# Performance work log

Hardware: AMD Instinct MI355X
Metric: run time of the kernel (lower is better)

## Reference

```python
import jax, jax.numpy as jnp
import numpy as np

B, N, S, D = 32, 128, 64, 512
MAX_LEN = 5000


def make_pe(d_model, max_len):
    pos = np.arange(max_len, dtype=np.float32)[:, None]
    div = np.exp(np.arange(0, d_model, 2, dtype=np.float32) * (-np.log(10000.0) / d_model))
    pe = np.zeros((max_len, d_model), dtype=np.float32)
    pe[:, 0::2] = np.sin(pos * div)
    pe[:, 1::2] = np.cos(pos * div)
    return jnp.asarray(pe)


def setup_inputs() -> dict:
    key = jax.random.key(0)
    ks = jax.random.split(key, 16)
    s1 = 1.0 / np.sqrt(D)
    s2 = 1.0 / np.sqrt(2 * D)
    inp = {
        "x": jax.random.normal(ks[0], (B, N), jnp.float32),
        "timesteps": jax.random.randint(ks[1], (B,), 0, 1000),
        "fusion_feat": jax.random.normal(ks[2], (B, D), jnp.float32),
        "tar_image_feat": jax.random.normal(ks[3], (B, N, S, D), jnp.float32),
        "pe": make_pe(D, MAX_LEN),
        # torch Linear weights are [out, in]
        "Wq": jax.random.normal(ks[4], (D, D), jnp.float32) * s1,
        "Wk": jax.random.normal(ks[5], (D, D), jnp.float32) * s1,
        "Wv": jax.random.normal(ks[6], (D, D), jnp.float32) * s1,
        "Wp": jax.random.normal(ks[7], (D, D), jnp.float32) * s1,
        "bp": jnp.zeros((D,), jnp.float32),
        "Wt1": jax.random.normal(ks[8], (D, D), jnp.float32) * s1,
        "bt1": jnp.zeros((D,), jnp.float32),
        "Wt2": jax.random.normal(ks[9], (D, D), jnp.float32) * s1,
        "bt2": jnp.zeros((D,), jnp.float32),
        "Wd1": jax.random.normal(ks[10], (2 * D, 2 * D), jnp.float32) * s2,
        "bd1": jnp.zeros((2 * D,), jnp.float32),
        "Wd2": jax.random.normal(ks[11], (1, 2 * D), jnp.float32) * s2,
        "bd2": jnp.zeros((1,), jnp.float32),
    }
    return inp


def reference(x, timesteps, fusion_feat, tar_image_feat, pe,
              Wq, Wk, Wv, Wp, bp, Wt1, bt1, Wt2, bt2, Wd1, bd1, Wd2, bd2):
    # timestep embedding: pe[timesteps] -> [B, D], then 2-layer SiLU MLP (eval mode: dropout off)
    cond = jax.nn.silu(pe[timesteps] @ Wt1.T + bt1) @ Wt2.T + bt2  # [B, D]

    # similarity argmax over S tokens, then gather best token per (b, n)
    sim = jnp.einsum('bd,bnsd->bns', fusion_feat, tar_image_feat)  # [B, N, S]
    best = jnp.argmax(sim, axis=-1)                                # [B, N]
    tif = jnp.take_along_axis(tar_image_feat, best[:, :, None, None], axis=2)[:, :, 0, :]  # [B, N, D]

    # single-vector attention over N candidates
    q = (fusion_feat + cond) @ Wq.T                  # [B, D]
    k = (tif + cond[:, None, :]) @ Wk.T              # [B, N, D]
    v = (tif + cond[:, None, :]) @ Wv.T              # [B, N, D]
    w = jax.nn.softmax(jnp.einsum('bd,bnd->bn', q, k) + x, axis=-1)  # [B, N]
    new_emb = jnp.einsum('bn,bnd->bd', w, v) @ Wp.T + bp             # [B, D]

    # MLP decode over concat [new_emb (broadcast), tif]
    emb = jnp.concatenate([jnp.broadcast_to(new_emb[:, None, :], tif.shape), tif], axis=-1)  # [B, N, 2D]
    h = jax.nn.relu(emb @ Wd1.T + bd1)
    p = (h @ Wd2.T + bd2)[..., 0] + w                # [B, N]

    # sort descending along N
    return -jnp.sort(-p, axis=1)
```

## Files before the change

kernel.cpp:

```cpp
#include <hip/hip_runtime.h>
#include <hip/hip_bf16.h>
#include <math.h>


#define BB 32
#define NN 128
#define SS 64
#define DD 512

typedef __attribute__((ext_vector_type(8))) short short8;
typedef __attribute__((ext_vector_type(4))) float f32x4;

__device__ __forceinline__ ushort f2bf(float f) {
    unsigned u = __float_as_uint(f);
    unsigned r = (u + 0x7fffu + ((u >> 16) & 1u)) >> 16;
    return (ushort)r;
}

__device__ __forceinline__ unsigned* flag_at(unsigned* fl, int b, int s) {
    return fl + (size_t)(b * 8 + s) * 16;
}
__device__ __forceinline__ void flag_add(unsigned* f) {
    __syncthreads();
    if (threadIdx.x == 0)
        __hip_atomic_fetch_add(f, 1u, __ATOMIC_RELEASE, __HIP_MEMORY_SCOPE_AGENT);
}
__device__ __forceinline__ void flag_wait(unsigned* f, unsigned target) {
    if (threadIdx.x == 0) {
        while (__hip_atomic_load(f, __ATOMIC_RELAXED, __HIP_MEMORY_SCOPE_AGENT) < target)
            __builtin_amdgcn_s_sleep(4);
        __builtin_amdgcn_fence(__ATOMIC_ACQUIRE, "agent");
    }
    __syncthreads();
}

__global__ __launch_bounds__(256) void k_init(unsigned* __restrict__ flags) {
    flags[blockIdx.x * 256 + threadIdx.x] = 0u;
}

__device__ __forceinline__ void wave_dot512x4(
    const float* __restrict__ w, size_t ldw, float4 xa, float4 xb,
    int lane, float out[4]) {
    float4 ra[4], rb[4];
#pragma unroll
    for (int r = 0; r < 4; ++r) {
        const float4* row = reinterpret_cast<const float4*>(w + (size_t)r * ldw);
        ra[r] = row[lane * 2];
        rb[r] = row[lane * 2 + 1];
    }
#pragma unroll
    for (int r = 0; r < 4; ++r) {
        float s = ra[r].x * xa.x + ra[r].y * xa.y + ra[r].z * xa.z + ra[r].w * xa.w
                + rb[r].x * xb.x + rb[r].y * xb.y + rb[r].z * xb.z + rb[r].w * xb.w;
#pragma unroll
        for (int off = 32; off; off >>= 1) s += __shfl_xor(s, off);
        out[r] = s;
    }
}

__global__ __launch_bounds__(256) void bmv(
    const float* __restrict__ W, int ldw, const float* __restrict__ bias,
    const float* __restrict__ Xa, float* __restrict__ Y, int R, int act) {
    __shared__ __align__(16) float xl[DD];
    int b = blockIdx.y, tid = threadIdx.x, lane = tid & 63, wave = tid >> 6;
    const float* src = Xa + (size_t)b * DD;
    for (int i = tid; i < DD; i += 256) xl[i] = src[i];
    __syncthreads();
    float4 xa = reinterpret_cast<const float4*>(xl)[lane * 2];
    float4 xb = reinterpret_cast<const float4*>(xl)[lane * 2 + 1];
    int j0 = blockIdx.x * 16 + wave * 4;
    float s[4];
    wave_dot512x4(W + (size_t)j0 * ldw, ldw, xa, xb, lane, s);
    if (lane < 4) {
        int j = j0 + lane;
        float v = s[lane];
        if (bias) v += bias[j];
        if (act == 1) v = v / (1.f + expf(-v));
        Y[(size_t)b * R + j] = v;
    }
}

__global__ __launch_bounds__(256) void k2_fused(
    const int* __restrict__ ts, const float* __restrict__ pe,
    const float* __restrict__ fusion, const float* __restrict__ tif,
    const float* __restrict__ Wt1, const float* __restrict__ bt1,
    const float* __restrict__ Wt2, const float* __restrict__ bt2,
    const float* __restrict__ Wq, const float* __restrict__ Wk,
    const float* __restrict__ Wd1, ushort* __restrict__ Wb,
    float* __restrict__ h, float* __restrict__ q,
    float* __restrict__ cond, float* __restrict__ qk,
    float* __restrict__ tif_best, ushort* __restrict__ abf,
    unsigned* __restrict__ flags) {
    __shared__ __align__(16) float xl[DD];
    __shared__ __align__(16) float paux[4][64];
    __shared__ float bv_s[4];
    __shared__ int bi_s[4];
    __shared__ int bidx_s;
    int blk = blockIdx.x, tid = threadIdx.x, lane = tid & 63, wave = tid >> 6;

    if (blk < 256) {
        int b = blk >> 3, part = blk & 7;
        int rows0 = part * 64;
        {
            const float* per = pe + (size_t)ts[b] * DD;
            for (int i = tid; i < DD; i += 256) xl[i] = per[i];
        }
        __syncthreads();
        {
            float4 xa = reinterpret_cast<const float4*>(xl)[lane * 2];
            float4 xb = reinterpret_cast<const float4*>(xl)[lane * 2 + 1];
            for (int j0 = rows0 + wave * 16; j0 < rows0 + wave * 16 + 16; j0 += 4) {
                float s[4];
                wave_dot512x4(Wt1 + (size_t)j0 * DD, DD, xa, xb, lane, s);
                if (lane < 4) {
                    float v = s[lane] + bt1[j0 + lane];
                    h[(size_t)b * DD + j0 + lane] = v / (1.f + expf(-v));
                }
            }
        }
        flag_add(flag_at(flags, b, 0));
        flag_wait(flag_at(flags, b, 0), 8);
        for (int i = tid; i < DD; i += 256) xl[i] = h[(size_t)b * DD + i];
        __syncthreads();
        {
            float4 xa = reinterpret_cast<const float4*>(xl)[lane * 2];
            float4 xb = reinterpret_cast<const float4*>(xl)[lane * 2 + 1];
            for (int j0 = rows0 + wave * 16; j0 < rows0 + wave * 16 + 16; j0 += 4) {
                float s[4];
                wave_dot512x4(Wt2 + (size_t)j0 * DD, DD, xa, xb, lane, s);
                if (lane < 4)
                    cond[(size_t)b * DD + j0 + lane] = s[lane] + bt2[j0 + lane];
            }
        }
        flag_add(flag_at(flags, b, 1));
        flag_wait(flag_at(flags, b, 1), 8);
        for (int i = tid; i < DD; i += 256)
            xl[i] = fusion[(size_t)b * DD + i] + cond[(size_t)b * DD + i];
        __syncthreads();
        {
            float4 xa = reinterpret_cast<const float4*>(xl)[lane * 2];
            float4 xb = reinterpret_cast<const float4*>(xl)[lane * 2 + 1];
            for (int j0 = rows0 + wave * 16; j0 < rows0 + wave * 16 + 16; j0 += 4) {
                float s[4];
                wave_dot512x4(Wq + (size_t)j0 * DD, DD, xa, xb, lane, s);
                if (lane < 4) q[(size_t)b * DD + j0 + lane] = s[lane];
            }
        }
        flag_add(flag_at(flags, b, 2));
        flag_wait(flag_at(flags, b, 2), 8);
        for (int i = tid; i < DD; i += 256) xl[i] = q[(size_t)b * DD + i];
        __syncthreads();
        {
            int c0 = part * 64;
            float p = 0.f;
            for (int j = wave * 128; j < wave * 128 + 128; ++j)
                p += xl[j] * Wk[(size_t)j * DD + c0 + lane];
            paux[wave][lane] = p;
            __syncthreads();
            if (tid < 64)
                qk[(size_t)b * DD + c0 + tid] =
                    paux[0][tid] + paux[1][tid] + paux[2][tid] + paux[3][tid];
        }
        return;
    }

    int bn = blk - 256, b = bn >> 7;
    if (bn < 1024) {
        int idx = (bn * 256 + tid) * 2;
        int r = idx >> 9, k = idx & 511;
        float2 v = *reinterpret_cast<const float2*>(Wd1 + (size_t)r * 1024 + 512 + k);
        ushort2 o = {f2bf(v.x), f2bf(v.y)};
        *reinterpret_cast<ushort2*>(Wb + (size_t)r * 512 + k) = o;
    }
    for (int i = tid; i < DD; i += 256) xl[i] = fusion[(size_t)b * DD + i];
    __syncthreads();
    float4 xa = reinterpret_cast<const float4*>(xl)[lane * 2];
    float4 xb = reinterpret_cast<const float4*>(xl)[lane * 2 + 1];
    const float* base = tif + (size_t)bn * SS * DD;
    float bv = -INFINITY;
    int bi = 0;
    for (int s0 = wave * 16; s0 < wave * 16 + 16; s0 += 4) {
        float sv[4];
        wave_dot512x4(base + (size_t)s0 * DD, DD, xa, xb, lane, sv);
#pragma unroll
        for (int r = 0; r < 4; ++r)
            if (sv[r] > bv) { bv = sv[r]; bi = s0 + r; }
    }
    if (lane == 0) { bv_s[wave] = bv; bi_s[wave] = bi; }
    __syncthreads();
    if (tid == 0) {
        float v = bv_s[0]; int i0 = bi_s[0];
        for (int w = 1; w < 4; w++)
            if (bv_s[w] > v) { v = bv_s[w]; i0 = bi_s[w]; }
        bidx_s = i0;
    }
    __syncthreads();
    const float* src = base + (size_t)bidx_s * DD;
    for (int i = tid; i < DD; i += 256) {
        float vv = src[i];
        tif_best[(size_t)bn * DD + i] = vv;
        abf[(size_t)bn * DD + i] = f2bf(vv);
    }
}

__global__ __launch_bounds__(256) void k_vsum(
    const float* __restrict__ qk, const float* __restrict__ x,
    const float* __restrict__ tif_best, const float* __restrict__ cond,
    float* __restrict__ wout, float* __restrict__ vsum) {
    __shared__ __align__(16) float qkl[DD];
    __shared__ float wl[NN];
    __shared__ float redm[2], reds[2];
    int b = blockIdx.y, tid = threadIdx.x, lane = tid & 63, wave = tid >> 6;
    for (int i = tid; i < DD; i += 256) qkl[i] = qk[(size_t)b * DD + i];
    __syncthreads();
    {
        float4 xa = reinterpret_cast<const float4*>(qkl)[lane * 2];
        float4 xb = reinterpret_cast<const float4*>(qkl)[lane * 2 + 1];
        for (int n0 = wave * 32; n0 < wave * 32 + 32; n0 += 4) {
            float s[4];
            wave_dot512x4(tif_best + ((size_t)(b * NN + n0)) * DD, DD, xa, xb, lane, s);
            if (lane < 4) wl[n0 + lane] = s[lane] + x[b * NN + n0 + lane];
        }
    }
    __syncthreads();
    float v = 0.f;
    if (tid < NN) {
        v = wl[tid];
        float m = v;
#pragma unroll
        for (int off = 32; off; off >>= 1) m = fmaxf(m, __shfl_xor(m, off));
        if (lane == 0) redm[wave] = m;
    }
    __syncthreads();
    float m = fmaxf(redm[0], redm[1]);
    float e = 0.f;
    if (tid < NN) {
        e = expf(v - m);
        float s = e;
#pragma unroll
        for (int off = 32; off; off >>= 1) s += __shfl_xor(s, off);
        if (lane == 0) reds[wave] = s;
    }
    __syncthreads();
    if (tid < NN) wl[tid] = e;
    __syncthreads();
    float inv = 1.f / (reds[0] + reds[1]);
    if (blockIdx.x == 0 && tid < NN) wout[b * NN + tid] = wl[tid] * inv;
    int d = blockIdx.x * 256 + tid;
    const float* base = tif_best + (size_t)b * NN * DD + d;
    float s = 0.f;
#pragma unroll 8
    for (int n = 0; n < NN; n++) s += wl[n] * base[(size_t)n * DD];
    vsum[(size_t)b * DD + d] = s * inv + cond[(size_t)b * DD + d];
}

__global__ __launch_bounds__(256) void k4_mfma(
    const ushort* __restrict__ Abf, const ushort* __restrict__ Wb,
    const float* __restrict__ Wd1, const float* __restrict__ bd1,
    const float* __restrict__ ne, const float* __restrict__ Wd2,
    float* __restrict__ p_part) {
    __shared__ ushort aS[2][128 * 64];
    __shared__ ushort bS[2][128 * 64];
    __shared__ __align__(16) float nel[DD];
    __shared__ float uloc[128];
    int tid = threadIdx.x, l = tid & 63, w = tid >> 6;
    int m0 = blockIdx.x * 128, n0 = blockIdx.y * 128;
    int b = blockIdx.x;
    int wm = w >> 1, wn = w & 1;

    for (int i = tid; i < DD; i += 256) nel[i] = ne[(size_t)b * DD + i];
    __syncthreads();
    float4 na = reinterpret_cast<const float4*>(nel)[l * 2];
    float4 nb = reinterpret_cast<const float4*>(nel)[l * 2 + 1];

#define STAGE(K0, BUF)                                                         \
    {                                                                          \
        _Pragma("unroll") for (int i = 0; i < 4; ++i) {                        \
            int L = i * 4096 + w * 1024 + l * 16;                              \
            int row = L >> 7;                                                  \
            int bo = L & 127;                                                  \
            int sb = bo ^ ((row & 7) << 4);                                    \
            const ushort* ga = Abf + (size_t)(m0 + row) * DD + (K0) + (sb >> 1); \
            const ushort* gb = Wb + (size_t)(n0 + row) * DD + (K0) + (sb >> 1);  \
            __builtin_amdgcn_global_load_lds(                                  \
                (const __attribute__((address_space(1))) void*)ga,             \
                (__attribute__((address_space(3))) void*)(aS[BUF] + i * 2048 + w * 512), \
                16, 0, 0);                                                     \
            __builtin_amdgcn_global_load_lds(                                  \
                (const __attribute__((address_space(1))) void*)gb,             \
                (__attribute__((address_space(3))) void*)(bS[BUF] + i * 2048 + w * 512), \
                16, 0, 0);                                                     \
        }                                                                      \
    }

    STAGE(0, 0);
    for (int j0 = 0; j0 < 32; j0 += 4) {
        int r = w * 32 + j0;
        float s[4];
        wave_dot512x4(Wd1 + (size_t)(n0 + r) * 1024, 1024, na, nb, l, s);
        if (l < 4) uloc[r + l] = s[l] + bd1[n0 + r + l];
    }
    __syncthreads();

    f32x4 acc[4][4];
#pragma unroll
    for (int i = 0; i < 4; i++)
#pragma unroll
        for (int j = 0; j < 4; j++) acc[i][j] = (f32x4){0.f, 0.f, 0.f, 0.f};

    int cur = 0;
    for (int k0 = 0; k0 < DD; k0 += 64) {
        if (k0 + 64 < DD) STAGE(k0 + 64, cur ^ 1);
#pragma unroll
        for (int kk = 0; kk < 2; ++kk) {
            short8 af[4], bf[4];
#pragma unroll
            for (int f = 0; f < 4; ++f) {
                int ra = wm * 64 + f * 16 + (l & 15);
                int boa = (((l >> 4) * 16 + kk * 64)) ^ ((ra & 7) << 4);
                af[f] = *reinterpret_cast<const short8*>(&aS[cur][ra * 64 + (boa >> 1)]);
                int rb = wn * 64 + f * 16 + (l & 15);
                int bob = (((l >> 4) * 16 + kk * 64)) ^ ((rb & 7) << 4);
                bf[f] = *reinterpret_cast<const short8*>(&bS[cur][rb * 64 + (bob >> 1)]);
            }
#pragma unroll
            for (int fm = 0; fm < 4; ++fm)
#pragma unroll
                for (int fn = 0; fn < 4; ++fn)
                    acc[fm][fn] = __builtin_amdgcn_mfma_f32_16x16x32_bf16(
                        af[fm], bf[fn], acc[fm][fn], 0, 0, 0);
        }
        __syncthreads();
        cur ^= 1;
    }
#undef STAGE
#pragma unroll
    for (int fm = 0; fm < 4; ++fm) {
#pragma unroll
        for (int reg = 0; reg < 4; ++reg) {
            float pp = 0.f;
#pragma unroll
            for (int fn = 0; fn < 4; ++fn) {
                int rl = wn * 64 + fn * 16 + (l & 15);
                float hh = acc[fm][fn][reg] + uloc[rl];
                if (hh > 0.f) pp += Wd2[n0 + rl] * hh;
            }
#pragma unroll
            for (int off = 1; off < 16; off <<= 1) pp += __shfl_xor(pp, off);
            if ((l & 15) == 0) {
                int m = m0 + wm * 64 + fm * 16 + (l >> 4) * 4 + reg;
                p_part[(size_t)m * 16 + blockIdx.y * 2 + wn] = pp;
            }
        }
    }
}

__global__ __launch_bounds__(128) void k5_sort(
    const float* __restrict__ p_part, const float* __restrict__ wout,
    const float* __restrict__ bd2, float* __restrict__ out) {
    __shared__ float v[NN];
    int b = blockIdx.x, tid = threadIdx.x;
    int bn = b * NN + tid;
    float s = bd2[0] + wout[bn];
#pragma unroll
    for (int c = 0; c < 16; c++) s += p_part[(size_t)bn * 16 + c];
    v[tid] = s;
    __syncthreads();
    for (int k = 2; k <= NN; k <<= 1) {
        for (int j = k >> 1; j > 0; j >>= 1) {
            int ixj = tid ^ j;
            if (ixj > tid) {
                float a = v[tid], bb2 = v[ixj];
                bool desc = (tid & k) == 0;
                if (desc ? (a < bb2) : (a > bb2)) { v[tid] = bb2; v[ixj] = a; }
            }
            __syncthreads();
        }
    }
    out[bn] = v[tid];
}

extern "C" void kernel_launch(void* const* d_in, const int* in_sizes, int n_in,
                              void* d_out, int out_size, void* d_ws, size_t ws_size,
                              hipStream_t stream) {
    const float* x      = (const float*)d_in[0];
    const int*   ts     = (const int*)d_in[1];
    const float* fusion = (const float*)d_in[2];
    const float* tif    = (const float*)d_in[3];
    const float* pe     = (const float*)d_in[4];
    const float* Wq     = (const float*)d_in[5];
    const float* Wk     = (const float*)d_in[6];
    const float* Wv     = (const float*)d_in[7];
    const float* Wp     = (const float*)d_in[8];
    const float* bp     = (const float*)d_in[9];
    const float* Wt1    = (const float*)d_in[10];
    const float* bt1    = (const float*)d_in[11];
    const float* Wt2    = (const float*)d_in[12];
    const float* bt2    = (const float*)d_in[13];
    const float* Wd1    = (const float*)d_in[14];
    const float* bd1    = (const float*)d_in[15];
    const float* Wd2    = (const float*)d_in[16];
    const float* bd2    = (const float*)d_in[17];

    float* ws = (float*)d_ws;
    float* cond     = ws;
    float* qk       = cond + 16384;
    float* h        = qk + 16384;
    float* q        = h + 16384;
    float* wout     = q + 16384;
    float* vsum     = wout + 4096;
    float* ve       = vsum + 16384;
    float* ne       = ve + 16384;
    float* p_part   = ne + 16384;
    float* tif_best = p_part + 65536;
    ushort* Abf     = (ushort*)(tif_best + 2097152);
    ushort* Wb      = Abf + 2097152;
    unsigned* flags = (unsigned*)(Wb + 524288);
    float* out = (float*)d_out;

    hipLaunchKernelGGL(k_init, dim3(16), dim3(256), 0, stream, flags);

    hipLaunchKernelGGL(k2_fused, dim3(256 + BB * NN), dim3(256), 0, stream,
                       ts, pe, fusion, tif, Wt1, bt1, Wt2, bt2, Wq, Wk,
                       Wd1, Wb, h, q, cond, qk, tif_best, Abf, flags);

    hipLaunchKernelGGL(k_vsum, dim3(2, BB), dim3(256), 0, stream,
                       qk, x, tif_best, cond, wout, vsum);

    hipLaunchKernelGGL(bmv, dim3(32, BB), dim3(256), 0, stream,
                       Wv, DD, nullptr, vsum, ve, DD, 0);
    hipLaunchKernelGGL(bmv, dim3(32, BB), dim3(256), 0, stream,
                       Wp, DD, bp, ve, ne, DD, 0);

    hipLaunchKernelGGL(k4_mfma, dim3(32, 8), dim3(256), 0, stream,
                       Abf, Wb, Wd1, bd1, ne, Wd2, p_part);
    hipLaunchKernelGGL(k5_sort, dim3(BB), dim3(128), 0, stream,
                       p_part, wout, bd2, out);
}
```

Before: 205.0 us.

## Split head MLP into grid-barrier kernel and fuse attention tail with scores

```diff
diff --git a/kernel.cpp b/kernel.cpp
--- a/kernel.cpp
+++ b/kernel.cpp
@@ -17,25 +17,28 @@
     return (ushort)r;
 }
 
-__device__ __forceinline__ unsigned* flag_at(unsigned* fl, int b, int s) {
-    return fl + (size_t)(b * 8 + s) * 16;
-}
-__device__ __forceinline__ void flag_add(unsigned* f) {
-    __syncthreads();
-    if (threadIdx.x == 0)
-        __hip_atomic_fetch_add(f, 1u, __ATOMIC_RELEASE, __HIP_MEMORY_SCOPE_AGENT);
-}
-__device__ __forceinline__ void flag_wait(unsigned* f, unsigned target) {
+__device__ __forceinline__ void bar_sync(unsigned* base, int blk) {
+    __syncthreads();
     if (threadIdx.x == 0) {
-        while (__hip_atomic_load(f, __ATOMIC_RELAXED, __HIP_MEMORY_SCOPE_AGENT) < target)
-            __builtin_amdgcn_s_sleep(4);
+        unsigned* grp = base + (blk >> 5) * 16;
+        if (__hip_atomic_fetch_add(grp, 1u, __ATOMIC_ACQ_REL,
+                                   __HIP_MEMORY_SCOPE_AGENT) == 31u) {
+            if (__hip_atomic_fetch_add(base + 120, 1u, __ATOMIC_ACQ_REL,
+                                       __HIP_MEMORY_SCOPE_AGENT) == 7u) {
+                __hip_atomic_store(base + 124, 1u, __ATOMIC_RELEASE,
+                                   __HIP_MEMORY_SCOPE_AGENT);
+            }
+        }
+        while (__hip_atomic_load(base + 124, __ATOMIC_RELAXED,
+                                 __HIP_MEMORY_SCOPE_AGENT) == 0u)
+            __builtin_amdgcn_s_sleep(2);
         __builtin_amdgcn_fence(__ATOMIC_ACQUIRE, "agent");
     }
     __syncthreads();
 }
 
-__global__ __launch_bounds__(256) void k_init(unsigned* __restrict__ flags) {
-    flags[blockIdx.x * 256 + threadIdx.x] = 0u;
+__global__ __launch_bounds__(256) void k_init(unsigned* __restrict__ bars) {
+    for (int i = threadIdx.x; i < 5 * 128; i += 256) bars[i] = 0u;
 }
 
 __device__ __forceinline__ void wave_dot512x4(
@@ -58,113 +61,96 @@
     }
 }
 
-__global__ __launch_bounds__(256) void bmv(
-    const float* __restrict__ W, int ldw, const float* __restrict__ bias,
-    const float* __restrict__ Xa, float* __restrict__ Y, int R, int act) {
-    __shared__ __align__(16) float xl[DD];
-    int b = blockIdx.y, tid = threadIdx.x, lane = tid & 63, wave = tid >> 6;
-    const float* src = Xa + (size_t)b * DD;
-    for (int i = tid; i < DD; i += 256) xl[i] = src[i];
-    __syncthreads();
-    float4 xa = reinterpret_cast<const float4*>(xl)[lane * 2];
-    float4 xb = reinterpret_cast<const float4*>(xl)[lane * 2 + 1];
-    int j0 = blockIdx.x * 16 + wave * 4;
-    float s[4];
-    wave_dot512x4(W + (size_t)j0 * ldw, ldw, xa, xb, lane, s);
-    if (lane < 4) {
-        int j = j0 + lane;
-        float v = s[lane];
-        if (bias) v += bias[j];
-        if (act == 1) v = v / (1.f + expf(-v));
-        Y[(size_t)b * R + j] = v;
-    }
-}
-
-__global__ __launch_bounds__(256) void k2_fused(
+__global__ __launch_bounds__(256) void k_head(
     const int* __restrict__ ts, const float* __restrict__ pe,
-    const float* __restrict__ fusion, const float* __restrict__ tif,
+    const float* __restrict__ fusion,
     const float* __restrict__ Wt1, const float* __restrict__ bt1,
     const float* __restrict__ Wt2, const float* __restrict__ bt2,
     const float* __restrict__ Wq, const float* __restrict__ Wk,
+    float* __restrict__ h, float* __restrict__ cond,
+    float* __restrict__ q, float* __restrict__ qk,
+    unsigned* __restrict__ bars) {
+    __shared__ __align__(16) float xl[DD];
+    __shared__ float paux[4][64];
+    int blk = blockIdx.x, tid = threadIdx.x, lane = tid & 63, wave = tid >> 6;
+    int b = blk & 31, seg = blk >> 5;
+
+    {
+        const float* per = pe + (size_t)ts[b] * DD;
+        for (int i = tid; i < DD; i += 256) xl[i] = per[i];
+        __syncthreads();
+        float4 xa = reinterpret_cast<const float4*>(xl)[lane * 2];
+        float4 xb = reinterpret_cast<const float4*>(xl)[lane * 2 + 1];
+        for (int j0 = seg * 64 + wave * 16; j0 < seg * 64 + wave * 16 + 16; j0 += 4) {
+            float s[4];
+            wave_dot512x4(Wt1 + (size_t)j0 * DD, DD, xa, xb, lane, s);
+            if (lane < 4) {
+                float v = s[lane] + bt1[j0 + lane];
+                h[(size_t)b * DD + j0 + lane] = v / (1.f + expf(-v));
+            }
+        }
+    }
+    bar_sync(bars + 0 * 128, blk);
+
+    {
+        const float* src = h + (size_t)b * DD;
+        for (int i = tid; i < DD; i += 256) xl[i] = src[i];
+        __syncthreads();
+        float4 xa = reinterpret_cast<const float4*>(xl)[lane * 2];
+        float4 xb = reinterpret_cast<const float4*>(xl)[lane * 2 + 1];
+        for (int j0 = seg * 64 + wave * 16; j0 < seg * 64 + wave * 16 + 16; j0 += 4) {
+            float s[4];
+            wave_dot512x4(Wt2 + (size_t)j0 * DD, DD, xa, xb, lane, s);
+            if (lane < 4)
+                cond[(size_t)b * DD + j0 + lane] = s[lane] + bt2[j0 + lane];
+        }
+    }
+    bar_sync(bars + 1 * 128, blk);
+
+    {
+        for (int i = tid; i < DD; i += 256)
+            xl[i] = fusion[(size_t)b * DD + i] + cond[(size_t)b * DD + i];
+        __syncthreads();
+        float4 xa = reinterpret_cast<const float4*>(xl)[lane * 2];
+        float4 xb = reinterpret_cast<const float4*>(xl)[lane * 2 + 1];
+        for (int j0 = seg * 64 + wave * 16; j0 < seg * 64 + wave * 16 + 16; j0 += 4) {
+            float s[4];
+            wave_dot512x4(Wq + (size_t)j0 * DD, DD, xa, xb, lane, s);
+            if (lane < 4) q[(size_t)b * DD + j0 + lane] = s[lane];
+        }
+    }
+    bar_sync(bars + 2 * 128, blk);
+
+    {
+        const float* src = q + (size_t)b * DD;
+        for (int i = tid; i < DD; i += 256) xl[i] = src[i];
+        __syncthreads();
+        int c0 = seg * 64;
+        float p = 0.f;
+        for (int j = wave * 128; j < wave * 128 + 128; ++j)
+            p += xl[j] * Wk[(size_t)j * DD + c0 + lane];
+        paux[wave][lane] = p;
+        __syncthreads();
+        if (tid < 64)
+            qk[(size_t)b * DD + c0 + tid] =
+                paux[0][tid] + paux[1][tid] + paux[2][tid] + paux[3][tid];
+    }
+}
+
+__global__ __launch_bounds__(256) void k2_sim(
+    const float* __restrict__ fusion, const float* __restrict__ tif,
+    const float* __restrict__ x, const float* __restrict__ qk,
     const float* __restrict__ Wd1, ushort* __restrict__ Wb,
-    float* __restrict__ h, float* __restrict__ q,
-    float* __restrict__ cond, float* __restrict__ qk,
     float* __restrict__ tif_best, ushort* __restrict__ abf,
-    unsigned* __restrict__ flags) {
-    __shared__ __align__(16) float xl[DD];
-    __shared__ __align__(16) float paux[4][64];
+    float* __restrict__ score) {
+    __shared__ __align__(16) float fb[DD];
     __shared__ float bv_s[4];
     __shared__ int bi_s[4];
     __shared__ int bidx_s;
-    int blk = blockIdx.x, tid = threadIdx.x, lane = tid & 63, wave = tid >> 6;
-
-    if (blk < 256) {
-        int b = blk >> 3, part = blk & 7;
-        int rows0 = part * 64;
-        {
-            const float* per = pe + (size_t)ts[b] * DD;
-            for (int i = tid; i < DD; i += 256) xl[i] = per[i];
-        }
-        __syncthreads();
-        {
-            float4 xa = reinterpret_cast<const float4*>(xl)[lane * 2];
-            float4 xb = reinterpret_cast<const float4*>(xl)[lane * 2 + 1];
-            for (int j0 = rows0 + wave * 16; j0 < rows0 + wave * 16 + 16; j0 += 4) {
-                float s[4];
-                wave_dot512x4(Wt1 + (size_t)j0 * DD, DD, xa, xb, lane, s);
-                if (lane < 4) {
-                    float v = s[lane] + bt1[j0 + lane];
-                    h[(size_t)b * DD + j0 + lane] = v / (1.f + expf(-v));
-                }
-            }
-        }
-        flag_add(flag_at(flags, b, 0));
-        flag_wait(flag_at(flags, b, 0), 8);
-        for (int i = tid; i < DD; i += 256) xl[i] = h[(size_t)b * DD + i];
-        __syncthreads();
-        {
-            float4 xa = reinterpret_cast<const float4*>(xl)[lane * 2];
-            float4 xb = reinterpret_cast<const float4*>(xl)[lane * 2 + 1];
-            for (int j0 = rows0 + wave * 16; j0 < rows0 + wave * 16 + 16; j0 += 4) {
-                float s[4];
-                wave_dot512x4(Wt2 + (size_t)j0 * DD, DD, xa, xb, lane, s);
-                if (lane < 4)
-                    cond[(size_t)b * DD + j0 + lane] = s[lane] + bt2[j0 + lane];
-            }
-        }
-        flag_add(flag_at(flags, b, 1));
-        flag_wait(flag_at(flags, b, 1), 8);
-        for (int i = tid; i < DD; i += 256)
-            xl[i] = fusion[(size_t)b * DD + i] + cond[(size_t)b * DD + i];
-        __syncthreads();
-        {
-            float4 xa = reinterpret_cast<const float4*>(xl)[lane * 2];
-            float4 xb = reinterpret_cast<const float4*>(xl)[lane * 2 + 1];
-            for (int j0 = rows0 + wave * 16; j0 < rows0 + wave * 16 + 16; j0 += 4) {
-                float s[4];
-                wave_dot512x4(Wq + (size_t)j0 * DD, DD, xa, xb, lane, s);
-                if (lane < 4) q[(size_t)b * DD + j0 + lane] = s[lane];
-            }
-        }
-        flag_add(flag_at(flags, b, 2));
-        flag_wait(flag_at(flags, b, 2), 8);
-        for (int i = tid; i < DD; i += 256) xl[i] = q[(size_t)b * DD + i];
-        __syncthreads();
-        {
-            int c0 = part * 64;
-            float p = 0.f;
-            for (int j = wave * 128; j < wave * 128 + 128; ++j)
-                p += xl[j] * Wk[(size_t)j * DD + c0 + lane];
-            paux[wave][lane] = p;
-            __syncthreads();
-            if (tid < 64)
-                qk[(size_t)b * DD + c0 + tid] =
-                    paux[0][tid] + paux[1][tid] + paux[2][tid] + paux[3][tid];
-        }
-        return;
-    }
-
-    int bn = blk - 256, b = bn >> 7;
+    __shared__ float dred[4];
+    int bn = blockIdx.x, b = bn >> 7;
+    int tid = threadIdx.x, lane = tid & 63, wave = tid >> 6;
+
     if (bn < 1024) {
         int idx = (bn * 256 + tid) * 2;
         int r = idx >> 9, k = idx & 511;
@@ -172,10 +158,11 @@
         ushort2 o = {f2bf(v.x), f2bf(v.y)};
         *reinterpret_cast<ushort2*>(Wb + (size_t)r * 512 + k) = o;
     }
-    for (int i = tid; i < DD; i += 256) xl[i] = fusion[(size_t)b * DD + i];
-    __syncthreads();
-    float4 xa = reinterpret_cast<const float4*>(xl)[lane * 2];
-    float4 xb = reinterpret_cast<const float4*>(xl)[lane * 2 + 1];
+
+    for (int i = tid; i < DD; i += 256) fb[i] = fusion[(size_t)b * DD + i];
+    __syncthreads();
+    float4 xa = reinterpret_cast<const float4*>(fb)[lane * 2];
+    float4 xb = reinterpret_cast<const float4*>(fb)[lane * 2 + 1];
     const float* base = tif + (size_t)bn * SS * DD;
     float bv = -INFINITY;
     int bi = 0;
@@ -196,36 +183,39 @@
     }
     __syncthreads();
     const float* src = base + (size_t)bidx_s * DD;
+    const float* qkb = qk + (size_t)b * DD;
+    float local = 0.f;
     for (int i = tid; i < DD; i += 256) {
         float vv = src[i];
         tif_best[(size_t)bn * DD + i] = vv;
         abf[(size_t)bn * DD + i] = f2bf(vv);
-    }
-}
-
-__global__ __launch_bounds__(256) void k_vsum(
-    const float* __restrict__ qk, const float* __restrict__ x,
-    const float* __restrict__ tif_best, const float* __restrict__ cond,
-    float* __restrict__ wout, float* __restrict__ vsum) {
-    __shared__ __align__(16) float qkl[DD];
+        local += vv * qkb[i];
+    }
+#pragma unroll
+    for (int off = 32; off; off >>= 1) local += __shfl_xor(local, off);
+    if (lane == 0) dred[wave] = local;
+    __syncthreads();
+    if (tid == 0) score[bn] = dred[0] + dred[1] + dred[2] + dred[3] + x[bn];
+}
+
+__global__ __launch_bounds__(256) void k_tail(
+    const float* __restrict__ score, const float* __restrict__ tif_best,
+    const float* __restrict__ cond,
+    const float* __restrict__ Wv, const float* __restrict__ Wp,
+    const float* __restrict__ bp,
+    float* __restrict__ wout, float* __restrict__ vsum,
+    float* __restrict__ ve, float* __restrict__ ne,
+    unsigned* __restrict__ bars) {
+    __shared__ __align__(16) float xl[DD];
     __shared__ float wl[NN];
+    __shared__ float paux[4][64];
     __shared__ float redm[2], reds[2];
-    int b = blockIdx.y, tid = threadIdx.x, lane = tid & 63, wave = tid >> 6;
-    for (int i = tid; i < DD; i += 256) qkl[i] = qk[(size_t)b * DD + i];
-    __syncthreads();
-    {
-        float4 xa = reinterpret_cast<const float4*>(qkl)[lane * 2];
-        float4 xb = reinterpret_cast<const float4*>(qkl)[lane * 2 + 1];
-        for (int n0 = wave * 32; n0 < wave * 32 + 32; n0 += 4) {
-            float s[4];
-            wave_dot512x4(tif_best + ((size_t)(b * NN + n0)) * DD, DD, xa, xb, lane, s);
-            if (lane < 4) wl[n0 + lane] = s[lane] + x[b * NN + n0 + lane];
-        }
-    }
-    __syncthreads();
+    int blk = blockIdx.x, tid = threadIdx.x, lane = tid & 63, wave = tid >> 6;
+    int b = blk & 31, seg = blk >> 5;
+
     float v = 0.f;
     if (tid < NN) {
-        v = wl[tid];
+        v = score[b * NN + tid];
         float m = v;
 #pragma unroll
         for (int off = 32; off; off >>= 1) m = fmaxf(m, __shfl_xor(m, off));
@@ -242,16 +232,52 @@
         if (lane == 0) reds[wave] = s;
     }
     __syncthreads();
-    if (tid < NN) wl[tid] = e;
-    __syncthreads();
     float inv = 1.f / (reds[0] + reds[1]);
-    if (blockIdx.x == 0 && tid < NN) wout[b * NN + tid] = wl[tid] * inv;
-    int d = blockIdx.x * 256 + tid;
-    const float* base = tif_best + (size_t)b * NN * DD + d;
-    float s = 0.f;
-#pragma unroll 8
-    for (int n = 0; n < NN; n++) s += wl[n] * base[(size_t)n * DD];
-    vsum[(size_t)b * DD + d] = s * inv + cond[(size_t)b * DD + d];
+    if (tid < NN) wl[tid] = e * inv;
+    __syncthreads();
+    if (seg == 0 && tid < NN) wout[b * NN + tid] = wl[tid];
+    {
+        int d0 = seg * 64;
+        float p = 0.f;
+        const float* tb = tif_best + (size_t)b * NN * DD + d0 + lane;
+        for (int n = wave * 32; n < wave * 32 + 32; ++n)
+            p += wl[n] * tb[(size_t)n * DD];
+        paux[wave][lane] = p;
+        __syncthreads();
+        if (tid < 64)
+            vsum[(size_t)b * DD + d0 + tid] =
+                paux[0][tid] + paux[1][tid] + paux[2][tid] + paux[3][tid]
+                + cond[(size_t)b * DD + d0 + tid];
+    }
+    bar_sync(bars + 3 * 128, blk);
+
+    {
+        const float* src = vsum + (size_t)b * DD;
+        for (int i = tid; i < DD; i += 256) xl[i] = src[i];
+        __syncthreads();
+        float4 xa = reinterpret_cast<const float4*>(xl)[lane * 2];
+        float4 xb = reinterpret_cast<const float4*>(xl)[lane * 2 + 1];
+        for (int j0 = seg * 64 + wave * 16; j0 < seg * 64 + wave * 16 + 16; j0 += 4) {
+            float s[4];
+            wave_dot512x4(Wv + (size_t)j0 * DD, DD, xa, xb, lane, s);
+            if (lane < 4) ve[(size_t)b * DD + j0 + lane] = s[lane];
+        }
+    }
+    bar_sync(bars + 4 * 128, blk);
+
+    {
+        const float* src = ve + (size_t)b * DD;
+        for (int i = tid; i < DD; i += 256) xl[i] = src[i];
+        __syncthreads();
+        float4 xa = reinterpret_cast<const float4*>(xl)[lane * 2];
+        float4 xb = reinterpret_cast<const float4*>(xl)[lane * 2 + 1];
+        for (int j0 = seg * 64 + wave * 16; j0 < seg * 64 + wave * 16 + 16; j0 += 4) {
+            float s[4];
+            wave_dot512x4(Wp + (size_t)j0 * DD, DD, xa, xb, lane, s);
+            if (lane < 4)
+                ne[(size_t)b * DD + j0 + lane] = s[lane] + bp[j0 + lane];
+        }
+    }
 }
 
 __global__ __launch_bounds__(256) void k4_mfma(
@@ -407,7 +433,8 @@
     float* qk       = cond + 16384;
     float* h        = qk + 16384;
     float* q        = h + 16384;
-    float* wout     = q + 16384;
+    float* score    = q + 16384;
+    float* wout     = score + 4096;
     float* vsum     = wout + 4096;
     float* ve       = vsum + 16384;
     float* ne       = ve + 16384;
@@ -415,22 +442,21 @@
     float* tif_best = p_part + 65536;
     ushort* Abf     = (ushort*)(tif_best + 2097152);
     ushort* Wb      = Abf + 2097152;
-    unsigned* flags = (unsigned*)(Wb + 524288);
+    unsigned* bars  = (unsigned*)(Wb + 524288);
     float* out = (float*)d_out;
 
-    hipLaunchKernelGGL(k_init, dim3(16), dim3(256), 0, stream, flags);
-
-    hipLaunchKernelGGL(k2_fused, dim3(256 + BB * NN), dim3(256), 0, stream,
-                       ts, pe, fusion, tif, Wt1, bt1, Wt2, bt2, Wq, Wk,
-                       Wd1, Wb, h, q, cond, qk, tif_best, Abf, flags);
-
-    hipLaunchKernelGGL(k_vsum, dim3(2, BB), dim3(256), 0, stream,
-                       qk, x, tif_best, cond, wout, vsum);
-
-    hipLaunchKernelGGL(bmv, dim3(32, BB), dim3(256), 0, stream,
-                       Wv, DD, nullptr, vsum, ve, DD, 0);
-    hipLaunchKernelGGL(bmv, dim3(32, BB), dim3(256), 0, stream,
-                       Wp, DD, bp, ve, ne, DD, 0);
+    hipLaunchKernelGGL(k_init, dim3(1), dim3(256), 0, stream, bars);
+
+    hipLaunchKernelGGL(k_head, dim3(256), dim3(256), 0, stream,
+                       ts, pe, fusion, Wt1, bt1, Wt2, bt2, Wq, Wk,
+                       h, cond, q, qk, bars);
+
+    hipLaunchKernelGGL(k2_sim, dim3(BB * NN), dim3(256), 0, stream,
+                       fusion, tif, x, qk, Wd1, Wb, tif_best, Abf, score);
+
+    hipLaunchKernelGGL(k_tail, dim3(256), dim3(256), 0, stream,
+                       score, tif_best, cond, Wv, Wp, bp,
+                       wout, vsum, ve, ne, bars);
 
     hipLaunchKernelGGL(k4_mfma, dim3(32, 8), dim3(256), 0, stream,
                        Abf, Wb, Wd1, bd1, ne, Wd2, p_part);
```

Result: slower. 238.0 us (+16.1%).
